# Kernel optimization log

Hardware: AMD Instinct MI355X
Metric: run time of the kernel (lower is better)

## Reference

```python
import jax, jax.numpy as jnp
import numpy as np

DIM = 768
NUM_HEADS = 12
HEAD_DIM = DIM // NUM_HEADS
SCALE = HEAD_DIM ** -0.5


def setup_inputs() -> dict:
    key = jax.random.key(0)
    ks = jax.random.split(key, 9)
    B, N = 2, 4096
    s = DIM ** -0.5
    return {
        "query": jax.random.normal(ks[0], (B, N, DIM), jnp.float32),
        "key": jax.random.normal(ks[1], (B, N, DIM), jnp.float32),
        "value": jax.random.normal(ks[2], (B, N, DIM), jnp.float32),
        "Wq": jax.random.normal(ks[3], (DIM, DIM), jnp.float32) * s,
        "Wk": jax.random.normal(ks[4], (DIM, DIM), jnp.float32) * s,
        "bk": jax.random.normal(ks[5], (DIM,), jnp.float32) * 0.02,
        "Wv": jax.random.normal(ks[6], (DIM, DIM), jnp.float32) * s,
        "Wp": jax.random.normal(ks[7], (DIM, DIM), jnp.float32) * s,
        "bp": jax.random.normal(ks[8], (DIM,), jnp.float32) * 0.02,
    }


def reference(query, key, value, Wq, Wk, bk, Wv, Wp, bp):
    B, Nq, C = query.shape
    Nk = key.shape[1]
    H, D = NUM_HEADS, HEAD_DIM
    # QKV projections (qv_bias=False -> no bias on q, v; k has bias)
    q = (query @ Wq.T).reshape(B, Nq, H, D).transpose(0, 2, 1, 3)  # [B,H,Nq,D]
    k = (key @ Wk.T + bk).reshape(B, Nk, H, D).transpose(0, 2, 1, 3)
    v = (value @ Wv.T).reshape(B, Nk, H, D).transpose(0, 2, 1, 3)
    # non-standard: exact GELU applied to K before QK^T
    k = jax.nn.gelu(k, approximate=False)
    attn = jnp.einsum("bhqd,bhkd->bhqk", q, k) * SCALE
    attn = jax.nn.softmax(attn, axis=-1)
    x = jnp.einsum("bhqk,bhkd->bhqd", attn, v)
    x = x.transpose(0, 2, 1, 3).reshape(B, Nq, C)
    return x @ Wp.T + bp
```

## Files before the change

### kernel.cpp

```cpp
#include <hip/hip_runtime.h>
#include <hip/hip_bf16.h>


#define DIM 768
#define NH 12
#define HD 64
#define NTOK 4096
#define WELEM 589824u
#define TELEM 6291456u

typedef short bf16x8 __attribute__((ext_vector_type(8)));
typedef float floatx4 __attribute__((ext_vector_type(4)));
typedef unsigned short us4 __attribute__((ext_vector_type(4)));

__device__ __forceinline__ float bf2f(unsigned short u) {
    union { unsigned int i; float f; } v; v.i = ((unsigned int)u) << 16; return v.f;
}
__device__ __forceinline__ unsigned short f2bf(float f) {
    union { float f; unsigned int i; } v; v.f = f;
    unsigned int r = v.i + 0x7fffu + ((v.i >> 16) & 1u);
    return (unsigned short)(r >> 16);
}
__device__ __forceinline__ unsigned int packbf(float a, float b) {
    union { float f; unsigned int i; } ua, ub; ua.f = a; ub.f = b;
    unsigned int ra = ua.i + 0x7fffu + ((ua.i >> 16) & 1u);
    unsigned int rb = ub.i + 0x7fffu + ((ub.i >> 16) & 1u);
    return __builtin_amdgcn_perm(rb, ra, 0x07060302);
}
__device__ __forceinline__ void gl2lds16(const unsigned short* g, unsigned short* l) {
    __builtin_amdgcn_global_load_lds(
        (const __attribute__((address_space(1))) unsigned int*)g,
        (__attribute__((address_space(3))) unsigned int*)l, 16, 0, 0);
}
__device__ __forceinline__ bf16x8 ld8_f32_to_bf16(const float* p) {
    floatx4 f0 = *(const floatx4*)p;
    floatx4 f1 = *(const floatx4*)(p + 4);
    bf16x8 o;
    o[0] = (short)f2bf(f0[0]); o[1] = (short)f2bf(f0[1]);
    o[2] = (short)f2bf(f0[2]); o[3] = (short)f2bf(f0[3]);
    o[4] = (short)f2bf(f1[0]); o[5] = (short)f2bf(f1[1]);
    o[6] = (short)f2bf(f1[2]); o[7] = (short)f2bf(f1[3]);
    return o;
}

#if __has_builtin(__builtin_amdgcn_exp2f)
#define EXPFN(x) __builtin_amdgcn_exp2f(x)
#define QSCALE 0.18033688011f
#else
#define EXPFN(x) __expf(x)
#define QSCALE 0.125f
#endif

__global__ __launch_bounds__(256) void cvt_w(
    const float* __restrict__ a, const float* __restrict__ b,
    const float* __restrict__ c, const float* __restrict__ d,
    unsigned short* __restrict__ dst)
{
    size_t i = ((size_t)blockIdx.x * 256 + threadIdx.x) * 8;
    const float* s; size_t off;
    if (i < WELEM)            { s = a; off = i; }
    else if (i < 2u * WELEM)  { s = b; off = i - WELEM; }
    else if (i < 3u * WELEM)  { s = c; off = i - 2u * WELEM; }
    else                      { s = d; off = i - 3u * WELEM; }
    *(bf16x8*)(dst + i) = ld8_f32_to_bf16(s + off);
}

__global__ __launch_bounds__(256) void cvt_in(
    const float* __restrict__ a, const float* __restrict__ b,
    const float* __restrict__ c, unsigned short* __restrict__ dst)
{
    size_t i = ((size_t)blockIdx.x * 256 + threadIdx.x) * 8;
    const float* s; size_t off;
    if (i < TELEM)            { s = a; off = i; }
    else if (i < 2u * TELEM)  { s = b; off = i - TELEM; }
    else                      { s = c; off = i - 2u * TELEM; }
    *(bf16x8*)(dst + i) = ld8_f32_to_bf16(s + off);
}

template <int A_IS_BF16>
__device__ __forceinline__ void gemm128(
    const void* __restrict__ Av, const unsigned short* __restrict__ W,
    const float* __restrict__ bias, void* __restrict__ Cv,
    int has_bias, int do_gelu, int trans, int out_f32)
{
    __shared__ unsigned short As[128 * 64];
    __shared__ unsigned short Bs[128 * 64];
    const int m0 = blockIdx.x * 128, n0 = blockIdx.y * 128;
    const int tid = threadIdx.x;
    const int w = tid >> 6, l = tid & 63;
    const int g = l >> 4, r16 = l & 15;
    const int wm = w >> 1, wn = w & 1;
    const int ro = l >> 3, c = l & 7;
    const int cswz = ((c ^ ro) & 7) * 8;

    floatx4 acc[4][4];
#pragma unroll
    for (int i = 0; i < 4; i++)
#pragma unroll
        for (int j = 0; j < 4; j++) acc[i][j] = (floatx4){0.f, 0.f, 0.f, 0.f};

    for (int k0 = 0; k0 < DIM; k0 += 64) {
#pragma unroll
        for (int q = 0; q < 4; q++) {
            int rbase = w * 32 + q * 8;
            if (A_IS_BF16) {
                gl2lds16((const unsigned short*)Av + (size_t)(m0 + rbase + ro) * DIM + k0 + cswz,
                         As + rbase * 64);
            } else {
                bf16x8 a = ld8_f32_to_bf16((const float*)Av + (size_t)(m0 + rbase + ro) * DIM + k0 + c * 8);
                *(bf16x8*)(As + (rbase + ro) * 64 + cswz) = a;
            }
            gl2lds16(W + (size_t)(n0 + rbase + ro) * DIM + k0 + cswz, Bs + rbase * 64);
        }
        __syncthreads();

#pragma unroll
        for (int kk = 0; kk < 2; kk++) {
            bf16x8 af[4], bfr[4];
            int x = r16 & 7;
#pragma unroll
            for (int i = 0; i < 4; i++)
                af[i] = *(const bf16x8*)(As + (wm * 64 + i * 16 + r16) * 64 + (((kk * 4 + g) ^ x) * 8));
#pragma unroll
            for (int j = 0; j < 4; j++)
                bfr[j] = *(const bf16x8*)(Bs + (wn * 64 + j * 16 + r16) * 64 + (((kk * 4 + g) ^ x) * 8));
#pragma unroll
            for (int i = 0; i < 4; i++)
#pragma unroll
                for (int j = 0; j < 4; j++)
                    acc[i][j] = __builtin_amdgcn_mfma_f32_16x16x32_bf16(af[i], bfr[j], acc[i][j], 0, 0, 0);
        }
        __syncthreads();
    }

    if (trans) {
        unsigned short* C = (unsigned short*)Cv;
#pragma unroll
        for (int i = 0; i < 4; i++) {
            int m = m0 + wm * 64 + i * 16 + g * 4;
            int b = m >> 12, tloc = m & 4095;
#pragma unroll
            for (int j = 0; j < 4; j++) {
                int n = n0 + wn * 64 + j * 16 + r16;
                int h = n >> 6, d = n & 63;
                us4 pk;
                pk[0] = f2bf(acc[i][j][0]); pk[1] = f2bf(acc[i][j][1]);
                pk[2] = f2bf(acc[i][j][2]); pk[3] = f2bf(acc[i][j][3]);
                *(us4*)(C + ((size_t)(b * NH + h) * 64 + d) * NTOK + tloc) = pk;
            }
        }
    } else {
#pragma unroll
        for (int i = 0; i < 4; i++)
#pragma unroll
            for (int j = 0; j < 4; j++) {
                int n = n0 + wn * 64 + j * 16 + r16;
                float bv = has_bias ? bias[n] : 0.f;
#pragma unroll
                for (int r = 0; r < 4; r++) {
                    int m = m0 + wm * 64 + i * 16 + g * 4 + r;
                    float v = acc[i][j][r] + bv;
                    if (do_gelu) v = 0.5f * v * (1.f + erff(v * 0.70710678118f));
                    if (out_f32) ((float*)Cv)[(size_t)m * DIM + n] = v;
                    else ((unsigned short*)Cv)[(size_t)m * DIM + n] = f2bf(v);
                }
            }
    }
}

template <int A_IS_BF16>
__global__ __launch_bounds__(256) void qkv_gemm(
    const void* __restrict__ q_in, const void* __restrict__ k_in,
    const void* __restrict__ v_in,
    const unsigned short* __restrict__ Wq, const unsigned short* __restrict__ Wk,
    const unsigned short* __restrict__ Wv, const float* __restrict__ bk,
    unsigned short* __restrict__ Qo, unsigned short* __restrict__ Ko,
    unsigned short* __restrict__ Vto)
{
    int z = blockIdx.z;
    const void* A = (z == 0) ? q_in : (z == 1) ? k_in : v_in;
    const unsigned short* W = (z == 0) ? Wq : (z == 1) ? Wk : Wv;
    unsigned short* C = (z == 0) ? Qo : (z == 1) ? Ko : Vto;
    gemm128<A_IS_BF16>(A, W, bk, C, z == 1, z == 1, z == 2, 0);
}

__global__ __launch_bounds__(256) void out_gemm(
    const unsigned short* __restrict__ X, const unsigned short* __restrict__ Wp,
    const float* __restrict__ bp, float* __restrict__ out)
{
    gemm128<1>(X, Wp, bp, out, 1, 0, 0, 1);
}

__device__ __forceinline__ int swzf(int R) { return (R & 7) ^ ((R >> 2) & 6); }

__global__ __launch_bounds__(128, 2) void attn_kernel(
    const unsigned short* __restrict__ Q, const unsigned short* __restrict__ K,
    const unsigned short* __restrict__ Vt, unsigned short* __restrict__ X)
{
    __shared__ unsigned short Ks[64 * 64];
    __shared__ unsigned short Vs[64 * 64];
    const int qt = blockIdx.x, bh = blockIdx.y;
    const int b = bh / NH, h = bh % NH;
    const int tid = threadIdx.x;
    const int w = tid >> 6, l = tid & 63;
    const int g = l >> 4, r16 = l & 15;
    const int tokbase = b * NTOK;

    bf16x8 qfr[4][2];
#pragma unroll
    for (int qfi = 0; qfi < 4; qfi++) {
        int qrow = tokbase + qt * 128 + w * 64 + qfi * 16 + r16;
#pragma unroll
        for (int kk = 0; kk < 2; kk++) {
            bf16x8 t = *(const bf16x8*)(Q + (size_t)qrow * DIM + h * HD + kk * 32 + g * 8);
#pragma unroll
            for (int j = 0; j < 8; j++)
                t[j] = (short)f2bf(bf2f((unsigned short)t[j]) * QSCALE);
            qfr[qfi][kk] = t;
        }
    }

    int koff[4][2], voff[4][2];
#pragma unroll
    for (int ct = 0; ct < 4; ct++) {
        int krow = (ct >> 1) * 32 + (r16 >> 2) * 8 + (ct & 1) * 4 + (r16 & 3);
#pragma unroll
        for (int kk = 0; kk < 2; kk++)
            koff[ct][kk] = krow * 64 + (((kk * 4 + g) ^ swzf(krow)) * 8);
    }
#pragma unroll
    for (int dt = 0; dt < 4; dt++) {
        int vrow = dt * 16 + r16;
#pragma unroll
        for (int c = 0; c < 2; c++)
            voff[dt][c] = vrow * 64 + (((c * 4 + g) ^ swzf(vrow)) * 8);
    }

    int soff[8];
    const int srl = l >> 3, scc = l & 7;
    const int sstride = (w == 0) ? DIM : NTOK;
#pragma unroll
    for (int i = 0; i < 8; i++) {
        int row = i * 8 + srl;
        soff[i] = row * sstride + ((scc ^ swzf(row)) * 8);
    }
    const unsigned short* Kbase = K + (size_t)tokbase * DIM + h * HD;
    const unsigned short* Vbase = Vt + (size_t)bh * 64 * NTOK;

    floatx4 o[4][4];
#pragma unroll
    for (int qfi = 0; qfi < 4; qfi++)
#pragma unroll
        for (int dt = 0; dt < 4; dt++) o[qfi][dt] = (floatx4){0.f, 0.f, 0.f, 0.f};
    float lsum[4] = {0.f, 0.f, 0.f, 0.f};

    for (int kt = 0; kt < NTOK / 64; kt++) {
        if (w == 0) {
            const unsigned short* p = Kbase + (size_t)kt * 64 * DIM;
#pragma unroll
            for (int i = 0; i < 8; i++) gl2lds16(p + soff[i], Ks + i * 512);
        } else {
            const unsigned short* p = Vbase + kt * 64;
#pragma unroll
            for (int i = 0; i < 8; i++) gl2lds16(p + soff[i], Vs + i * 512);
        }
        __syncthreads();

        bf16x8 kr[4][2], vr[4][2];
#pragma unroll
        for (int ct = 0; ct < 4; ct++)
#pragma unroll
            for (int kk = 0; kk < 2; kk++)
                kr[ct][kk] = *(const bf16x8*)(Ks + koff[ct][kk]);
#pragma unroll
        for (int dt = 0; dt < 4; dt++)
#pragma unroll
            for (int c = 0; c < 2; c++)
                vr[dt][c] = *(const bf16x8*)(Vs + voff[dt][c]);

#pragma unroll
        for (int qfi = 0; qfi < 4; qfi++) {
            floatx4 s[4];
#pragma unroll
            for (int ct = 0; ct < 4; ct++) {
                floatx4 z = (floatx4){0.f, 0.f, 0.f, 0.f};
                z = __builtin_amdgcn_mfma_f32_16x16x32_bf16(kr[ct][0], qfr[qfi][0], z, 0, 0, 0);
                s[ct] = __builtin_amdgcn_mfma_f32_16x16x32_bf16(kr[ct][1], qfr[qfi][1], z, 0, 0, 0);
            }
            float ls = 0.f;
#pragma unroll
            for (int ct = 0; ct < 4; ct++)
#pragma unroll
                for (int r = 0; r < 4; r++) {
                    float p = EXPFN(s[ct][r]);
                    s[ct][r] = p;
                    ls += p;
                }
            lsum[qfi] += ls;

            unsigned int pk[4][2];
#pragma unroll
            for (int ct = 0; ct < 4; ct++) {
                pk[ct][0] = packbf(s[ct][0], s[ct][1]);
                pk[ct][1] = packbf(s[ct][2], s[ct][3]);
            }
#pragma unroll
            for (int c = 0; c < 2; c++) {
                union { unsigned int u[4]; bf16x8 v; } bf;
                bf.u[0] = pk[2 * c][0]; bf.u[1] = pk[2 * c][1];
                bf.u[2] = pk[2 * c + 1][0]; bf.u[3] = pk[2 * c + 1][1];
#pragma unroll
                for (int dt = 0; dt < 4; dt++)
                    o[qfi][dt] = __builtin_amdgcn_mfma_f32_16x16x32_bf16(vr[dt][c], bf.v, o[qfi][dt], 0, 0, 0);
            }
        }
        __syncthreads();
    }

#pragma unroll
    for (int qfi = 0; qfi < 4; qfi++) {
        lsum[qfi] += __shfl_xor(lsum[qfi], 16, 64);
        lsum[qfi] += __shfl_xor(lsum[qfi], 32, 64);
    }

#pragma unroll
    for (int qfi = 0; qfi < 4; qfi++) {
        float inv = 1.f / lsum[qfi];
        int tok = tokbase + qt * 128 + w * 64 + qfi * 16 + r16;
#pragma unroll
        for (int dt = 0; dt < 4; dt++) {
            us4 pkv;
            pkv[0] = f2bf(o[qfi][dt][0] * inv);
            pkv[1] = f2bf(o[qfi][dt][1] * inv);
            pkv[2] = f2bf(o[qfi][dt][2] * inv);
            pkv[3] = f2bf(o[qfi][dt][3] * inv);
            *(us4*)(X + (size_t)tok * DIM + h * HD + dt * 16 + g * 4) = pkv;
        }
    }
}

extern "C" void kernel_launch(void* const* d_in, const int* in_sizes, int n_in,
                              void* d_out, int out_size, void* d_ws, size_t ws_size,
                              hipStream_t stream) {
    const float* query = (const float*)d_in[0];
    const float* key   = (const float*)d_in[1];
    const float* value = (const float*)d_in[2];
    const float* Wq    = (const float*)d_in[3];
    const float* Wk    = (const float*)d_in[4];
    const float* bk    = (const float*)d_in[5];
    const float* Wv    = (const float*)d_in[6];
    const float* Wp    = (const float*)d_in[7];
    const float* bp    = (const float*)d_in[8];
    float* out = (float*)d_out;

    unsigned short* ws = (unsigned short*)d_ws;
    unsigned short* Wqb = ws;
    unsigned short* Wkb = Wqb + WELEM;
    unsigned short* Wvb = Wkb + WELEM;
    unsigned short* Wpb = Wvb + WELEM;
    unsigned short* Qp  = Wpb + WELEM;
    unsigned short* Kp  = Qp + TELEM;
    unsigned short* Vtp = Kp + TELEM;
    unsigned short* Xp  = Vtp + TELEM;
    unsigned short* Qbf = Xp + TELEM;
    unsigned short* Kbf = Qbf + TELEM;
    unsigned short* Vbf = Kbf + TELEM;

    const size_t need_full = ((size_t)4 * WELEM + 7 * TELEM) * 2;
    const bool full = ws_size >= need_full;

    cvt_w<<<dim3(4 * WELEM / 8 / 256), 256, 0, stream>>>(Wq, Wk, Wv, Wp, Wqb);
    if (full) {
        cvt_in<<<dim3(3 * TELEM / 8 / 256), 256, 0, stream>>>(query, key, value, Qbf);
        qkv_gemm<1><<<dim3(64, 6, 3), 256, 0, stream>>>(Qbf, Kbf, Vbf, Wqb, Wkb, Wvb, bk, Qp, Kp, Vtp);
    } else {
        qkv_gemm<0><<<dim3(64, 6, 3), 256, 0, stream>>>(query, key, value, Wqb, Wkb, Wvb, bk, Qp, Kp, Vtp);
    }
    attn_kernel<<<dim3(32, 24), 128, 0, stream>>>(Qp, Kp, Vtp, Xp);
    out_gemm<<<dim3(64, 6), 256, 0, stream>>>(Xp, Wpb, bp, out);
}
```

Baseline: 353.6 us.

## Split attention key range across two wave pairs and merge partial outputs in LDS

The attention kernel grows from 128 to 256 threads. Two extra waves process a second 64-key tile each iteration, halving the key-loop trip count, and all four waves cooperatively load K and V tiles into two LDS buffers. After the loop the second pair writes its fp32 partial outputs and row sums to shared memory, and the first pair adds them and normalizes. This raises per-block parallelism and latency hiding without a running max. In exchange it adds a reduction step through LDS, extra shared memory, and higher register pressure under launch bounds of 4 blocks per unit.

```diff
diff --git a/kernel.cpp b/kernel.cpp
--- a/kernel.cpp
+++ b/kernel.cpp
@@ -193,23 +193,29 @@
 
 __device__ __forceinline__ int swzf(int R) { return (R & 7) ^ ((R >> 2) & 6); }
 
-__global__ __launch_bounds__(128, 2) void attn_kernel(
+__global__ __launch_bounds__(256, 4) void attn_kernel(
     const unsigned short* __restrict__ Q, const unsigned short* __restrict__ K,
     const unsigned short* __restrict__ Vt, unsigned short* __restrict__ X)
 {
-    __shared__ unsigned short Ks[64 * 64];
-    __shared__ unsigned short Vs[64 * 64];
+    __shared__ unsigned short Smem[4 * 64 * 64];
+    __shared__ float Lx[2][64];
+    unsigned short* Ks0 = Smem;
+    unsigned short* Vs0 = Smem + 4096;
+    unsigned short* Ks1 = Smem + 8192;
+    unsigned short* Vs1 = Smem + 12288;
+
     const int qt = blockIdx.x, bh = blockIdx.y;
     const int b = bh / NH, h = bh % NH;
     const int tid = threadIdx.x;
     const int w = tid >> 6, l = tid & 63;
     const int g = l >> 4, r16 = l & 15;
+    const int wq = w & 1, wk = w >> 1;
     const int tokbase = b * NTOK;
 
     bf16x8 qfr[4][2];
 #pragma unroll
     for (int qfi = 0; qfi < 4; qfi++) {
-        int qrow = tokbase + qt * 128 + w * 64 + qfi * 16 + r16;
+        int qrow = tokbase + qt * 128 + wq * 64 + qfi * 16 + r16;
 #pragma unroll
         for (int kk = 0; kk < 2; kk++) {
             bf16x8 t = *(const bf16x8*)(Q + (size_t)qrow * DIM + h * HD + kk * 32 + g * 8);
@@ -220,6 +226,8 @@
         }
     }
 
+    const unsigned short* myKs = wk ? Ks1 : Ks0;
+    const unsigned short* myVs = wk ? Vs1 : Vs0;
     int koff[4][2], voff[4][2];
 #pragma unroll
     for (int ct = 0; ct < 4; ct++) {
@@ -236,9 +244,11 @@
             voff[dt][c] = vrow * 64 + (((c * 4 + g) ^ swzf(vrow)) * 8);
     }
 
+    unsigned short* sdst = (w == 0) ? Ks0 : (w == 1) ? Vs0 : (w == 2) ? Ks1 : Vs1;
+    const int isV = w & 1;
+    const int sstride = isV ? NTOK : DIM;
     int soff[8];
     const int srl = l >> 3, scc = l & 7;
-    const int sstride = (w == 0) ? DIM : NTOK;
 #pragma unroll
     for (int i = 0; i < 8; i++) {
         int row = i * 8 + srl;
@@ -254,16 +264,12 @@
         for (int dt = 0; dt < 4; dt++) o[qfi][dt] = (floatx4){0.f, 0.f, 0.f, 0.f};
     float lsum[4] = {0.f, 0.f, 0.f, 0.f};
 
-    for (int kt = 0; kt < NTOK / 64; kt++) {
-        if (w == 0) {
-            const unsigned short* p = Kbase + (size_t)kt * 64 * DIM;
-#pragma unroll
-            for (int i = 0; i < 8; i++) gl2lds16(p + soff[i], Ks + i * 512);
-        } else {
-            const unsigned short* p = Vbase + kt * 64;
-#pragma unroll
-            for (int i = 0; i < 8; i++) gl2lds16(p + soff[i], Vs + i * 512);
-        }
+    for (int kt = 0; kt < NTOK / 128; kt++) {
+        int keyoff = kt * 128 + (w >> 1) * 64;
+        const unsigned short* p = isV ? (Vbase + keyoff)
+                                      : (Kbase + (size_t)keyoff * DIM);
+#pragma unroll
+        for (int i = 0; i < 8; i++) gl2lds16(p + soff[i], sdst + i * 512);
         __syncthreads();
 
         bf16x8 kr[4][2], vr[4][2];
@@ -271,12 +277,12 @@
         for (int ct = 0; ct < 4; ct++)
 #pragma unroll
             for (int kk = 0; kk < 2; kk++)
-                kr[ct][kk] = *(const bf16x8*)(Ks + koff[ct][kk]);
+                kr[ct][kk] = *(const bf16x8*)(myKs + koff[ct][kk]);
 #pragma unroll
         for (int dt = 0; dt < 4; dt++)
 #pragma unroll
             for (int c = 0; c < 2; c++)
-                vr[dt][c] = *(const bf16x8*)(Vs + voff[dt][c]);
+                vr[dt][c] = *(const bf16x8*)(myVs + voff[dt][c]);
 
 #pragma unroll
         for (int qfi = 0; qfi < 4; qfi++) {
@@ -292,9 +298,9 @@
             for (int ct = 0; ct < 4; ct++)
 #pragma unroll
                 for (int r = 0; r < 4; r++) {
-                    float p = EXPFN(s[ct][r]);
-                    s[ct][r] = p;
-                    ls += p;
+                    float p2 = EXPFN(s[ct][r]);
+                    s[ct][r] = p2;
+                    ls += p2;
                 }
             lsum[qfi] += ls;
 
@@ -323,18 +329,42 @@
         lsum[qfi] += __shfl_xor(lsum[qfi], 32, 64);
     }
 
-#pragma unroll
-    for (int qfi = 0; qfi < 4; qfi++) {
-        float inv = 1.f / lsum[qfi];
-        int tok = tokbase + qt * 128 + w * 64 + qfi * 16 + r16;
-#pragma unroll
-        for (int dt = 0; dt < 4; dt++) {
-            us4 pkv;
-            pkv[0] = f2bf(o[qfi][dt][0] * inv);
-            pkv[1] = f2bf(o[qfi][dt][1] * inv);
-            pkv[2] = f2bf(o[qfi][dt][2] * inv);
-            pkv[3] = f2bf(o[qfi][dt][3] * inv);
-            *(us4*)(X + (size_t)tok * DIM + h * HD + dt * 16 + g * 4) = pkv;
+    float* Opart = (float*)Smem;
+    if (w >= 2) {
+        float* P = Opart + wq * 4096;
+#pragma unroll
+        for (int qfi = 0; qfi < 4; qfi++)
+#pragma unroll
+            for (int dt = 0; dt < 4; dt++)
+                *(floatx4*)(P + (qfi * 4 + dt) * 256 + l * 4) = o[qfi][dt];
+        if (g == 0)
+#pragma unroll
+            for (int qfi = 0; qfi < 4; qfi++)
+                Lx[wq][qfi * 16 + r16] = lsum[qfi];
+    }
+    __syncthreads();
+    if (w < 2) {
+        const float* P = Opart + wq * 4096;
+#pragma unroll
+        for (int qfi = 0; qfi < 4; qfi++) {
+#pragma unroll
+            for (int dt = 0; dt < 4; dt++)
+                o[qfi][dt] += *(const floatx4*)(P + (qfi * 4 + dt) * 256 + l * 4);
+            lsum[qfi] += Lx[wq][qfi * 16 + r16];
+        }
+#pragma unroll
+        for (int qfi = 0; qfi < 4; qfi++) {
+            float inv = 1.f / lsum[qfi];
+            int tok = tokbase + qt * 128 + wq * 64 + qfi * 16 + r16;
+#pragma unroll
+            for (int dt = 0; dt < 4; dt++) {
+                us4 pkv;
+                pkv[0] = f2bf(o[qfi][dt][0] * inv);
+                pkv[1] = f2bf(o[qfi][dt][1] * inv);
+                pkv[2] = f2bf(o[qfi][dt][2] * inv);
+                pkv[3] = f2bf(o[qfi][dt][3] * inv);
+                *(us4*)(X + (size_t)tok * DIM + h * HD + dt * 16 + g * 4) = pkv;
+            }
         }
     }
 }
@@ -376,6 +406,6 @@
     } else {
         qkv_gemm<0><<<dim3(64, 6, 3), 256, 0, stream>>>(query, key, value, Wqb, Wkb, Wvb, bk, Qp, Kp, Vtp);
     }
-    attn_kernel<<<dim3(32, 24), 128, 0, stream>>>(Qp, Kp, Vtp, Xp);
+    attn_kernel<<<dim3(32, 24), 256, 0, stream>>>(Qp, Kp, Vtp, Xp);
     out_gemm<<<dim3(64, 6), 256, 0, stream>>>(Xp, Wpb, bp, out);
 }
```

After: 1.273 ms. 3.6x slower.

## Split attention over key halves and merge partial outputs

Applied to the files above, without the earlier changes.

Splits the key dimension of the attention kernel into two halves launched as separate blocks, doubling the grid from 768 to 1536 blocks so the GPU's compute units are better filled. Each half writes unnormalized fp32 partial outputs and row sums, and a new merge kernel adds them, normalizes and converts to bf16. This works without max-subtraction because the softmax uses a fixed exponent with no running max. The cost is an extra kernel launch plus about 50MB of fp32 partial traffic, and a larger workspace requirement with a fallback path when the workspace is too small.

```diff
diff --git a/kernel.cpp b/kernel.cpp
--- a/kernel.cpp
+++ b/kernel.cpp
@@ -8,6 +8,7 @@
 #define NTOK 4096
 #define WELEM 589824u
 #define TELEM 6291456u
+#define LELEM 196608u
 
 typedef short bf16x8 __attribute__((ext_vector_type(8)));
 typedef float floatx4 __attribute__((ext_vector_type(4)));
@@ -193,13 +194,16 @@
 
 __device__ __forceinline__ int swzf(int R) { return (R & 7) ^ ((R >> 2) & 6); }
 
+template <int SPLIT>
 __global__ __launch_bounds__(128, 2) void attn_kernel(
     const unsigned short* __restrict__ Q, const unsigned short* __restrict__ K,
-    const unsigned short* __restrict__ Vt, unsigned short* __restrict__ X)
+    const unsigned short* __restrict__ Vt, unsigned short* __restrict__ X,
+    float* __restrict__ Op, float* __restrict__ Lp)
 {
     __shared__ unsigned short Ks[64 * 64];
     __shared__ unsigned short Vs[64 * 64];
     const int qt = blockIdx.x, bh = blockIdx.y;
+    const int z = (SPLIT == 2) ? blockIdx.z : 0;
     const int b = bh / NH, h = bh % NH;
     const int tid = threadIdx.x;
     const int w = tid >> 6, l = tid & 63;
@@ -246,6 +250,7 @@
     }
     const unsigned short* Kbase = K + (size_t)tokbase * DIM + h * HD;
     const unsigned short* Vbase = Vt + (size_t)bh * 64 * NTOK;
+    const int key0 = z * (NTOK / SPLIT);
 
     floatx4 o[4][4];
 #pragma unroll
@@ -254,13 +259,14 @@
         for (int dt = 0; dt < 4; dt++) o[qfi][dt] = (floatx4){0.f, 0.f, 0.f, 0.f};
     float lsum[4] = {0.f, 0.f, 0.f, 0.f};
 
-    for (int kt = 0; kt < NTOK / 64; kt++) {
+    for (int kt = 0; kt < NTOK / (64 * SPLIT); kt++) {
+        int keyg = key0 + kt * 64;
         if (w == 0) {
-            const unsigned short* p = Kbase + (size_t)kt * 64 * DIM;
+            const unsigned short* p = Kbase + (size_t)keyg * DIM;
 #pragma unroll
             for (int i = 0; i < 8; i++) gl2lds16(p + soff[i], Ks + i * 512);
         } else {
-            const unsigned short* p = Vbase + kt * 64;
+            const unsigned short* p = Vbase + keyg;
 #pragma unroll
             for (int i = 0; i < 8; i++) gl2lds16(p + soff[i], Vs + i * 512);
         }
@@ -283,18 +289,18 @@
             floatx4 s[4];
 #pragma unroll
             for (int ct = 0; ct < 4; ct++) {
-                floatx4 z = (floatx4){0.f, 0.f, 0.f, 0.f};
-                z = __builtin_amdgcn_mfma_f32_16x16x32_bf16(kr[ct][0], qfr[qfi][0], z, 0, 0, 0);
-                s[ct] = __builtin_amdgcn_mfma_f32_16x16x32_bf16(kr[ct][1], qfr[qfi][1], z, 0, 0, 0);
+                floatx4 zz = (floatx4){0.f, 0.f, 0.f, 0.f};
+                zz = __builtin_amdgcn_mfma_f32_16x16x32_bf16(kr[ct][0], qfr[qfi][0], zz, 0, 0, 0);
+                s[ct] = __builtin_amdgcn_mfma_f32_16x16x32_bf16(kr[ct][1], qfr[qfi][1], zz, 0, 0, 0);
             }
             float ls = 0.f;
 #pragma unroll
             for (int ct = 0; ct < 4; ct++)
 #pragma unroll
                 for (int r = 0; r < 4; r++) {
-                    float p = EXPFN(s[ct][r]);
-                    s[ct][r] = p;
-                    ls += p;
+                    float p2 = EXPFN(s[ct][r]);
+                    s[ct][r] = p2;
+                    ls += p2;
                 }
             lsum[qfi] += ls;
 
@@ -323,20 +329,54 @@
         lsum[qfi] += __shfl_xor(lsum[qfi], 32, 64);
     }
 
-#pragma unroll
-    for (int qfi = 0; qfi < 4; qfi++) {
-        float inv = 1.f / lsum[qfi];
-        int tok = tokbase + qt * 128 + w * 64 + qfi * 16 + r16;
-#pragma unroll
-        for (int dt = 0; dt < 4; dt++) {
-            us4 pkv;
-            pkv[0] = f2bf(o[qfi][dt][0] * inv);
-            pkv[1] = f2bf(o[qfi][dt][1] * inv);
-            pkv[2] = f2bf(o[qfi][dt][2] * inv);
-            pkv[3] = f2bf(o[qfi][dt][3] * inv);
-            *(us4*)(X + (size_t)tok * DIM + h * HD + dt * 16 + g * 4) = pkv;
-        }
-    }
+    if (SPLIT == 2) {
+#pragma unroll
+        for (int qfi = 0; qfi < 4; qfi++) {
+            int tok = tokbase + qt * 128 + w * 64 + qfi * 16 + r16;
+#pragma unroll
+            for (int dt = 0; dt < 4; dt++)
+                *(floatx4*)(Op + (size_t)z * TELEM + (size_t)tok * DIM + h * HD + dt * 16 + g * 4) = o[qfi][dt];
+            if (g == 0)
+                Lp[((size_t)z * 24 + bh) * 4096 + qt * 128 + w * 64 + qfi * 16 + r16] = lsum[qfi];
+        }
+    } else {
+#pragma unroll
+        for (int qfi = 0; qfi < 4; qfi++) {
+            float inv = 1.f / lsum[qfi];
+            int tok = tokbase + qt * 128 + w * 64 + qfi * 16 + r16;
+#pragma unroll
+            for (int dt = 0; dt < 4; dt++) {
+                us4 pkv;
+                pkv[0] = f2bf(o[qfi][dt][0] * inv);
+                pkv[1] = f2bf(o[qfi][dt][1] * inv);
+                pkv[2] = f2bf(o[qfi][dt][2] * inv);
+                pkv[3] = f2bf(o[qfi][dt][3] * inv);
+                *(us4*)(X + (size_t)tok * DIM + h * HD + dt * 16 + g * 4) = pkv;
+            }
+        }
+    }
+}
+
+__global__ __launch_bounds__(256) void merge_kernel(
+    const float* __restrict__ Op, const float* __restrict__ Lp,
+    unsigned short* __restrict__ X)
+{
+    size_t i = ((size_t)blockIdx.x * 256 + threadIdx.x) * 4;
+    int c = (int)(i % DIM);
+    size_t tok = i / DIM;
+    int b = (int)(tok >> 12), tl = (int)(tok & 4095);
+    int h = c >> 6;
+    float l0 = Lp[((size_t)(b * NH + h)) * 4096 + tl];
+    float l1 = Lp[((size_t)24 + b * NH + h) * 4096 + tl];
+    float inv = 1.f / (l0 + l1);
+    floatx4 a = *(const floatx4*)(Op + i);
+    floatx4 d = *(const floatx4*)(Op + TELEM + i);
+    us4 pkv;
+    pkv[0] = f2bf((a[0] + d[0]) * inv);
+    pkv[1] = f2bf((a[1] + d[1]) * inv);
+    pkv[2] = f2bf((a[2] + d[2]) * inv);
+    pkv[3] = f2bf((a[3] + d[3]) * inv);
+    *(us4*)(X + i) = pkv;
 }
 
 extern "C" void kernel_launch(void* const* d_in, const int* in_sizes, int n_in,
@@ -362,20 +402,35 @@
     unsigned short* Kp  = Qp + TELEM;
     unsigned short* Vtp = Kp + TELEM;
     unsigned short* Xp  = Vtp + TELEM;
-    unsigned short* Qbf = Xp + TELEM;
+    unsigned short* tail = Xp + TELEM;
+
+    const size_t base_b = ((size_t)4 * WELEM + 4 * TELEM) * 2;
+    const size_t cvt_b  = (size_t)3 * TELEM * 2;
+    const size_t part_b = (size_t)2 * TELEM * 4 + (size_t)LELEM * 4;
+
+    bool cvt_ok, split_ok;
+    unsigned short* Qbf = tail;
+    float* Opart;
+    if (ws_size >= base_b + cvt_b + part_b)      { cvt_ok = true;  split_ok = true;  Opart = (float*)(tail + 3 * TELEM); }
+    else if (ws_size >= base_b + part_b)         { cvt_ok = false; split_ok = true;  Opart = (float*)tail; }
+    else if (ws_size >= base_b + cvt_b)          { cvt_ok = true;  split_ok = false; Opart = nullptr; }
+    else                                         { cvt_ok = false; split_ok = false; Opart = nullptr; }
+    float* Lpart = Opart ? Opart + (size_t)2 * TELEM : nullptr;
     unsigned short* Kbf = Qbf + TELEM;
     unsigned short* Vbf = Kbf + TELEM;
 
-    const size_t need_full = ((size_t)4 * WELEM + 7 * TELEM) * 2;
-    const bool full = ws_size >= need_full;
-
     cvt_w<<<dim3(4 * WELEM / 8 / 256), 256, 0, stream>>>(Wq, Wk, Wv, Wp, Wqb);
-    if (full) {
+    if (cvt_ok) {
         cvt_in<<<dim3(3 * TELEM / 8 / 256), 256, 0, stream>>>(query, key, value, Qbf);
         qkv_gemm<1><<<dim3(64, 6, 3), 256, 0, stream>>>(Qbf, Kbf, Vbf, Wqb, Wkb, Wvb, bk, Qp, Kp, Vtp);
     } else {
         qkv_gemm<0><<<dim3(64, 6, 3), 256, 0, stream>>>(query, key, value, Wqb, Wkb, Wvb, bk, Qp, Kp, Vtp);
     }
-    attn_kernel<<<dim3(32, 24), 128, 0, stream>>>(Qp, Kp, Vtp, Xp);
+    if (split_ok) {
+        attn_kernel<2><<<dim3(32, 24, 2), 128, 0, stream>>>(Qp, Kp, Vtp, nullptr, Opart, Lpart);
+        merge_kernel<<<dim3(TELEM / 4 / 256), 256, 0, stream>>>(Opart, Lpart, Xp);
+    } else {
+        attn_kernel<1><<<dim3(32, 24), 128, 0, stream>>>(Qp, Kp, Vtp, Xp, nullptr, nullptr);
+    }
     out_gemm<<<dim3(64, 6), 256, 0, stream>>>(Xp, Wpb, bp, out);
 }
```

Result: slower. 367.2 us (+3.8%).

## Double-buffer K/V tiles in attention and use packed bf16 conversion

Applied to the files above, without the earlier changes.

The attention kernel now keeps two LDS buffers for K and V tiles. It issues the async global-to-LDS load for the next tile right after reading the current tile into registers, and drops one barrier per iteration. This is meant to overlap memory latency with the MFMA and exp work. Float-to-bf16 packing across the kernels switches to the HIP __float22bfloat162_rn intrinsic, which may map to a packed conversion instruction. LDS use doubles, which could affect occupancy, and the correctness of the overlap depends on the compiler waiting for the async LDS loads before the barrier.

```diff
diff --git a/kernel.cpp b/kernel.cpp
--- a/kernel.cpp
+++ b/kernel.cpp
@@ -22,10 +22,8 @@
     return (unsigned short)(r >> 16);
 }
 __device__ __forceinline__ unsigned int packbf(float a, float b) {
-    union { float f; unsigned int i; } ua, ub; ua.f = a; ub.f = b;
-    unsigned int ra = ua.i + 0x7fffu + ((ua.i >> 16) & 1u);
-    unsigned int rb = ub.i + 0x7fffu + ((ub.i >> 16) & 1u);
-    return __builtin_amdgcn_perm(rb, ra, 0x07060302);
+    __hip_bfloat162 h = __float22bfloat162_rn(make_float2(a, b));
+    union { __hip_bfloat162 h; unsigned int u; } cv; cv.h = h; return cv.u;
 }
 __device__ __forceinline__ void gl2lds16(const unsigned short* g, unsigned short* l) {
     __builtin_amdgcn_global_load_lds(
@@ -35,12 +33,12 @@
 __device__ __forceinline__ bf16x8 ld8_f32_to_bf16(const float* p) {
     floatx4 f0 = *(const floatx4*)p;
     floatx4 f1 = *(const floatx4*)(p + 4);
-    bf16x8 o;
-    o[0] = (short)f2bf(f0[0]); o[1] = (short)f2bf(f0[1]);
-    o[2] = (short)f2bf(f0[2]); o[3] = (short)f2bf(f0[3]);
-    o[4] = (short)f2bf(f1[0]); o[5] = (short)f2bf(f1[1]);
-    o[6] = (short)f2bf(f1[2]); o[7] = (short)f2bf(f1[3]);
-    return o;
+    union { unsigned int u[4]; bf16x8 v; } o;
+    o.u[0] = packbf(f0[0], f0[1]);
+    o.u[1] = packbf(f0[2], f0[3]);
+    o.u[2] = packbf(f1[0], f1[1]);
+    o.u[3] = packbf(f1[2], f1[3]);
+    return o.v;
 }
 
 #if __has_builtin(__builtin_amdgcn_exp2f)
@@ -143,10 +141,10 @@
             for (int j = 0; j < 4; j++) {
                 int n = n0 + wn * 64 + j * 16 + r16;
                 int h = n >> 6, d = n & 63;
-                us4 pk;
-                pk[0] = f2bf(acc[i][j][0]); pk[1] = f2bf(acc[i][j][1]);
-                pk[2] = f2bf(acc[i][j][2]); pk[3] = f2bf(acc[i][j][3]);
-                *(us4*)(C + ((size_t)(b * NH + h) * 64 + d) * NTOK + tloc) = pk;
+                union { unsigned int u[2]; us4 v; } pk;
+                pk.u[0] = packbf(acc[i][j][0], acc[i][j][1]);
+                pk.u[1] = packbf(acc[i][j][2], acc[i][j][3]);
+                *(us4*)(C + ((size_t)(b * NH + h) * 64 + d) * NTOK + tloc) = pk.v;
             }
         }
     } else {
@@ -197,8 +195,8 @@
     const unsigned short* __restrict__ Q, const unsigned short* __restrict__ K,
     const unsigned short* __restrict__ Vt, unsigned short* __restrict__ X)
 {
-    __shared__ unsigned short Ks[64 * 64];
-    __shared__ unsigned short Vs[64 * 64];
+    __shared__ unsigned short Ks[2][64 * 64];
+    __shared__ unsigned short Vs[2][64 * 64];
     const int qt = blockIdx.x, bh = blockIdx.y;
     const int b = bh / NH, h = bh % NH;
     const int tid = threadIdx.x;
@@ -254,16 +252,15 @@
         for (int dt = 0; dt < 4; dt++) o[qfi][dt] = (floatx4){0.f, 0.f, 0.f, 0.f};
     float lsum[4] = {0.f, 0.f, 0.f, 0.f};
 
+    {
+        const unsigned short* p = (w == 0) ? Kbase : Vbase;
+        unsigned short* dst = (w == 0) ? Ks[0] : Vs[0];
+#pragma unroll
+        for (int i = 0; i < 8; i++) gl2lds16(p + soff[i], dst + i * 512);
+    }
+
     for (int kt = 0; kt < NTOK / 64; kt++) {
-        if (w == 0) {
-            const unsigned short* p = Kbase + (size_t)kt * 64 * DIM;
-#pragma unroll
-            for (int i = 0; i < 8; i++) gl2lds16(p + soff[i], Ks + i * 512);
-        } else {
-            const unsigned short* p = Vbase + kt * 64;
-#pragma unroll
-            for (int i = 0; i < 8; i++) gl2lds16(p + soff[i], Vs + i * 512);
-        }
+        const int cur = kt & 1;
         __syncthreads();
 
         bf16x8 kr[4][2], vr[4][2];
@@ -271,30 +268,39 @@
         for (int ct = 0; ct < 4; ct++)
 #pragma unroll
             for (int kk = 0; kk < 2; kk++)
-                kr[ct][kk] = *(const bf16x8*)(Ks + koff[ct][kk]);
+                kr[ct][kk] = *(const bf16x8*)(Ks[cur] + koff[ct][kk]);
 #pragma unroll
         for (int dt = 0; dt < 4; dt++)
 #pragma unroll
             for (int c = 0; c < 2; c++)
-                vr[dt][c] = *(const bf16x8*)(Vs + voff[dt][c]);
+                vr[dt][c] = *(const bf16x8*)(Vs[cur] + voff[dt][c]);
+
+        if (kt + 1 < NTOK / 64) {
+            int keyg = (kt + 1) * 64;
+            const unsigned short* p = (w == 0) ? (Kbase + (size_t)keyg * DIM)
+                                               : (Vbase + keyg);
+            unsigned short* dst = (w == 0) ? Ks[cur ^ 1] : Vs[cur ^ 1];
+#pragma unroll
+            for (int i = 0; i < 8; i++) gl2lds16(p + soff[i], dst + i * 512);
+        }
 
 #pragma unroll
         for (int qfi = 0; qfi < 4; qfi++) {
             floatx4 s[4];
 #pragma unroll
             for (int ct = 0; ct < 4; ct++) {
-                floatx4 z = (floatx4){0.f, 0.f, 0.f, 0.f};
-                z = __builtin_amdgcn_mfma_f32_16x16x32_bf16(kr[ct][0], qfr[qfi][0], z, 0, 0, 0);
-                s[ct] = __builtin_amdgcn_mfma_f32_16x16x32_bf16(kr[ct][1], qfr[qfi][1], z, 0, 0, 0);
+                floatx4 zz = (floatx4){0.f, 0.f, 0.f, 0.f};
+                zz = __builtin_amdgcn_mfma_f32_16x16x32_bf16(kr[ct][0], qfr[qfi][0], zz, 0, 0, 0);
+                s[ct] = __builtin_amdgcn_mfma_f32_16x16x32_bf16(kr[ct][1], qfr[qfi][1], zz, 0, 0, 0);
             }
             float ls = 0.f;
 #pragma unroll
             for (int ct = 0; ct < 4; ct++)
 #pragma unroll
                 for (int r = 0; r < 4; r++) {
-                    float p = EXPFN(s[ct][r]);
-                    s[ct][r] = p;
-                    ls += p;
+                    float p2 = EXPFN(s[ct][r]);
+                    s[ct][r] = p2;
+                    ls += p2;
                 }
             lsum[qfi] += ls;
 
@@ -314,7 +320,6 @@
                     o[qfi][dt] = __builtin_amdgcn_mfma_f32_16x16x32_bf16(vr[dt][c], bf.v, o[qfi][dt], 0, 0, 0);
             }
         }
-        __syncthreads();
     }
 
 #pragma unroll
@@ -329,12 +334,10 @@
         int tok = tokbase + qt * 128 + w * 64 + qfi * 16 + r16;
 #pragma unroll
         for (int dt = 0; dt < 4; dt++) {
-            us4 pkv;
-            pkv[0] = f2bf(o[qfi][dt][0] * inv);
-            pkv[1] = f2bf(o[qfi][dt][1] * inv);
-            pkv[2] = f2bf(o[qfi][dt][2] * inv);
-            pkv[3] = f2bf(o[qfi][dt][3] * inv);
-            *(us4*)(X + (size_t)tok * DIM + h * HD + dt * 16 + g * 4) = pkv;
+            union { unsigned int u[2]; us4 v; } pkv;
+            pkv.u[0] = packbf(o[qfi][dt][0] * inv, o[qfi][dt][1] * inv);
+            pkv.u[1] = packbf(o[qfi][dt][2] * inv, o[qfi][dt][3] * inv);
+            *(us4*)(X + (size_t)tok * DIM + h * HD + dt * 16 + g * 4) = pkv.v;
         }
     }
 }
@@ -366,11 +369,12 @@
     unsigned short* Kbf = Qbf + TELEM;
     unsigned short* Vbf = Kbf + TELEM;
 
-    const size_t need_full = ((size_t)4 * WELEM + 7 * TELEM) * 2;
-    const bool full = ws_size >= need_full;
+    const size_t base_b = ((size_t)4 * WELEM + 4 * TELEM) * 2;
+    const size_t cvt_b  = (size_t)3 * TELEM * 2;
+    const bool cvt_ok = ws_size >= base_b + cvt_b;
 
     cvt_w<<<dim3(4 * WELEM / 8 / 256), 256, 0, stream>>>(Wq, Wk, Wv, Wp, Wqb);
-    if (full) {
+    if (cvt_ok) {
         cvt_in<<<dim3(3 * TELEM / 8 / 256), 256, 0, stream>>>(query, key, value, Qbf);
         qkv_gemm<1><<<dim3(64, 6, 3), 256, 0, stream>>>(Qbf, Kbf, Vbf, Wqb, Wkb, Wvb, bk, Qp, Kp, Vtp);
     } else {
```

After: 333.4 us. -5.7%, faster.
